# Performance work log

Hardware: AMD Instinct MI355X
Metric: run time of the kernel (lower is better)

The kernel has to match this reference:

```python
import jax, jax.numpy as jnp
import numpy as np

B, L, D, F = 8, 1024, 256, 11
TEMP = D ** 0.5
LN_EPS = 1e-6


def setup_inputs() -> dict:
    key = jax.random.key(0)
    ks = jax.random.split(key, 14)
    mk = lambda k, s: jax.random.normal(k, s, dtype=jnp.float32)
    return {
        "q": mk(ks[0], (B, L, D)),
        "k": mk(ks[1], (B, L, D)),
        "v": mk(ks[2], (B, L, D)),
        "x": jax.random.uniform(ks[3], (B, L, F), dtype=jnp.float32),
        "inputs_lengths": jax.random.randint(ks[4], (B,), 512, L + 1),
        "w_qs": mk(ks[5], (D, D)) * 0.05,
        "w_ks": mk(ks[6], (D, D)) * 0.05,
        "w_vs": mk(ks[7], (D, D)) * 0.05,
        "w_qs2": mk(ks[8], (D, D)) * 0.05,
        "w_ks2": mk(ks[9], (D, D)) * 0.05,
        "w_fc": mk(ks[10], (D, D)) * 0.05,
        "feature_importance": mk(ks[11], (F,)) * 0.1,
        "ln_gamma": jnp.ones((D,), jnp.float32),
        "ln_beta": jnp.zeros((D,), jnp.float32),
    }


def reference(q, k, v, x, w_qs, w_ks, w_vs, w_qs2, w_ks2, w_fc,
              feature_importance, ln_gamma, ln_beta, inputs_lengths):
    lin = lambda a, w: jnp.einsum('bli,oi->blo', a, w)  # torch Linear: y = x W^T
    qp = lin(q, w_qs)
    kp = lin(k, w_ks)
    vp = lin(v, w_vs)
    q2 = lin(q, w_qs2)
    k2 = lin(k, w_ks2)

    # key-position validity mask [B, L]
    key_mask = jnp.arange(L)[None, :] < inputs_lengths[:, None]

    # FeatureSim: pairwise L1 feature distances weighted by feature_importance
    fd = jnp.abs(x[:, :, None, :] - x[:, None, :, :])           # [B,L,L,F]
    fa = jnp.einsum('bijf,f->bij', fd, feature_importance)      # [B,L,L]
    fa = jnp.where(key_mask[:, None, :], fa, -jnp.inf)          # pad_masking
    fa = jax.nn.softmax(fa, axis=-1)
    fa = jnp.nan_to_num(fa)                                     # nan -> 0 for fully-masked rows

    # dual-score attention with tanh activation (no row normalization)
    attn = jnp.einsum('bid,bjd->bij', qp / TEMP, kp)
    q2f = jnp.einsum('bij,bjd->bid', fa, q2)
    k2f = jnp.einsum('bij,bjd->bid', fa, k2)
    attn = attn + jnp.einsum('bid,bjd->bij', q2f / TEMP, k2f)
    zm = key_mask[:, None, :]
    attn = jnp.where(zm, attn, 0.0)                             # pad_zero_masking
    attn = jnp.tanh(attn)
    attn = jnp.where(zm, attn, 0.0)                             # pad_zero_masking (tanh(0)=0, kept for fidelity)

    out = jnp.einsum('bij,bjd->bid', attn, vp)
    out = lin(out, w_fc) + q                                    # dropout is identity at eval
    mu = jnp.mean(out, axis=-1, keepdims=True)
    var = jnp.var(out, axis=-1, keepdims=True)
    out = (out - mu) / jnp.sqrt(var + LN_EPS) * ln_gamma + ln_beta
    return (out, attn)
```

## Files before the change

### kernel.cpp

```cpp
#include <hip/hip_runtime.h>
#include <hip/hip_bf16.h>
#include <math.h>

typedef __hip_bfloat16 bf16;
typedef __bf16 bf16x8 __attribute__((ext_vector_type(8)));
typedef float  f32x4  __attribute__((ext_vector_type(4)));

#define NB 8
#define SL 1024
#define DD 256
#define NF 11
#define RPB 8

#define AS_G __attribute__((address_space(1)))
#define AS_L __attribute__((address_space(3)))

__device__ __forceinline__ bf16x8 ldfrag(const bf16* p) {
  return *reinterpret_cast<const bf16x8*>(p);
}
__device__ __forceinline__ bf16x8 ldfrag(const float* p) {
  const float4 a = *reinterpret_cast<const float4*>(p);
  const float4 b = *reinterpret_cast<const float4*>(p + 4);
  bf16x8 r;
  r[0] = (__bf16)a.x; r[1] = (__bf16)a.y; r[2] = (__bf16)a.z; r[3] = (__bf16)a.w;
  r[4] = (__bf16)b.x; r[5] = (__bf16)b.y; r[6] = (__bf16)b.z; r[7] = (__bf16)b.w;
  return r;
}
__device__ __forceinline__ unsigned short us(float f) {
  bf16 h = __float2bfloat16(f);
  return *reinterpret_cast<unsigned short*>(&h);
}
__device__ __forceinline__ float tanh_fast(float x) {
  return 1.f - 2.f / (__expf(2.f * x) + 1.f);
}

template<int R>
__device__ __forceinline__ void stage_t(const float* __restrict__ g, int ld,
                                        bf16* __restrict__ s, int tid) {
#pragma unroll
  for (int it = 0; it < R / 32; ++it) {
    const int cid = it * 256 + tid;
    const int row = cid >> 3, c16 = cid & 7;
    bf16x8 v = ldfrag(g + (size_t)row * ld + c16 * 8);
    *reinterpret_cast<bf16x8*>(s + row * 64 + ((c16 ^ (row & 7)) << 3)) = v;
  }
}
template<int R>
__device__ __forceinline__ void stage_t(const bf16* __restrict__ g, int ld,
                                        bf16* __restrict__ s, int tid) {
  const int wbase = tid & ~63;
#pragma unroll
  for (int it = 0; it < R / 32; ++it) {
    const int cid = it * 256 + tid;
    const int row = cid >> 3, sc = cid & 7;
    const int c16 = sc ^ (row & 7);
    const bf16* src = g + (size_t)row * ld + c16 * 8;
    bf16* dst = s + (size_t)(it * 256 + wbase) * 8;
    __builtin_amdgcn_global_load_lds((const AS_G void*)src, (AS_L void*)dst, 16, 0, 0);
  }
}

__device__ __forceinline__ void compute_128x128(const bf16* __restrict__ sA,
                                                const bf16* __restrict__ sB,
                                                int lane, int wave, f32x4 acc[4][4]) {
  const int n15 = lane & 15, quad = lane >> 4;
  const int wr = (wave >> 1) << 6, wc = (wave & 1) << 6;
#pragma unroll
  for (int kc = 0; kc < 2; ++kc) {
    const int c16 = kc * 4 + quad;
    bf16x8 aF[4], bF[4];
#pragma unroll
    for (int t = 0; t < 4; ++t) {
      const int ra = wr + t * 16 + n15;
      aF[t] = *reinterpret_cast<const bf16x8*>(sA + ra * 64 + ((c16 ^ (ra & 7)) << 3));
      const int rb = wc + t * 16 + n15;
      bF[t] = *reinterpret_cast<const bf16x8*>(sB + rb * 64 + ((c16 ^ (rb & 7)) << 3));
    }
#pragma unroll
    for (int ti = 0; ti < 4; ++ti)
#pragma unroll
      for (int tj = 0; tj < 4; ++tj)
        acc[ti][tj] = __builtin_amdgcn_mfma_f32_16x16x32_bf16(aF[ti], bF[tj], acc[ti][tj], 0, 0, 0);
  }
}

__device__ __forceinline__ void compute_32x256(const bf16* __restrict__ sA,
                                               const bf16* __restrict__ sB,
                                               int lane, int wave, f32x4 acc[2][4]) {
  const int n15 = lane & 15, quad = lane >> 4;
  const int wc = wave << 6;
#pragma unroll
  for (int kc = 0; kc < 2; ++kc) {
    const int c16 = kc * 4 + quad;
    bf16x8 aF[2], bF[4];
#pragma unroll
    for (int t = 0; t < 2; ++t) {
      const int ra = t * 16 + n15;
      aF[t] = *reinterpret_cast<const bf16x8*>(sA + ra * 64 + ((c16 ^ (ra & 7)) << 3));
    }
#pragma unroll
    for (int t = 0; t < 4; ++t) {
      const int rb = wc + t * 16 + n15;
      bF[t] = *reinterpret_cast<const bf16x8*>(sB + rb * 64 + ((c16 ^ (rb & 7)) << 3));
    }
#pragma unroll
    for (int ti = 0; ti < 2; ++ti)
#pragma unroll
      for (int tj = 0; tj < 4; ++tj)
        acc[ti][tj] = __builtin_amdgcn_mfma_f32_16x16x32_bf16(aF[ti], bF[tj], acc[ti][tj], 0, 0, 0);
  }
}

template<typename TA, typename TB>
__device__ __forceinline__ void gemm_128x128(const TA* __restrict__ A, int lda,
                                             const TB* __restrict__ B, int ldb, int K,
                                             bf16* s, int tid, f32x4 acc[4][4]) {
  const int lane = tid & 63, wave = tid >> 6;
  stage_t<128>(A, lda, s, tid);
  stage_t<128>(B, ldb, s + 8192, tid);
  int cur = 0;
  __syncthreads();
  for (int k0 = 0; k0 < K; k0 += 64) {
    bf16* sc0 = s + cur * 16384;
    if (k0 + 64 < K) {
      bf16* sn = s + (cur ^ 1) * 16384;
      stage_t<128>(A + k0 + 64, lda, sn, tid);
      stage_t<128>(B + k0 + 64, ldb, sn + 8192, tid);
    }
    compute_128x128(sc0, sc0 + 8192, lane, wave, acc);
    __syncthreads();
    cur ^= 1;
  }
}

__device__ __forceinline__ float wred_sum(float v) {
#pragma unroll
  for (int o = 32; o > 0; o >>= 1) v += __shfl_xor(v, o, 64);
  return v;
}

__global__ __launch_bounds__(256) void k_fawc(const float* __restrict__ x,
                                              const float* __restrict__ fi_g,
                                              const int* __restrict__ lens,
                                              const float* __restrict__ wfc,
                                              const float* __restrict__ wvs,
                                              bf16* __restrict__ fa,
                                              float* __restrict__ Wc)
{
  __shared__ __align__(16) float sx[SL * NF];
  __shared__ float sredS[4][RPB];
  const int tid = threadIdx.x, wave = tid >> 6;
  const int bid = blockIdx.x;
  if (bid >= NB * 128) {
    const int o0 = (bid - NB * 128) * 4, m = tid;
    const float* f0 = wfc + (size_t)o0 * DD;
    float a0 = 0.f, a1 = 0.f, a2 = 0.f, a3 = 0.f;
#pragma unroll 8
    for (int i = 0; i < DD; ++i) {
      const float wv = wvs[(size_t)i * DD + m];
      a0 += f0[i] * wv;
      a1 += f0[DD + i] * wv;
      a2 += f0[2 * DD + i] * wv;
      a3 += f0[3 * DD + i] * wv;
    }
    Wc[(size_t)(o0 + 0) * DD + m] = a0;
    Wc[(size_t)(o0 + 1) * DD + m] = a1;
    Wc[(size_t)(o0 + 2) * DD + m] = a2;
    Wc[(size_t)(o0 + 3) * DD + m] = a3;
    return;
  }
  const int b  = bid >> 7;
  const int i0 = (bid & 127) * RPB;
  {
    const float4* src = reinterpret_cast<const float4*>(x + (size_t)b * SL * NF);
    float4* dst = reinterpret_cast<float4*>(sx);
#pragma unroll
    for (int it = 0; it < 11; ++it) dst[it * 256 + tid] = src[it * 256 + tid];
  }
  float fiv[NF];
#pragma unroll
  for (int f = 0; f < NF; ++f) fiv[f] = fi_g[f];
  const int len = lens[b];
  __syncthreads();
  float xi[RPB][NF];
#pragma unroll
  for (int i = 0; i < RPB; ++i)
#pragma unroll
    for (int f = 0; f < NF; ++f) xi[i][f] = sx[(i0 + i) * NF + f];
  float e[RPB][4];
  float ps[RPB];
#pragma unroll
  for (int i = 0; i < RPB; ++i) ps[i] = 0.f;
#pragma unroll
  for (int t = 0; t < 4; ++t) {
    const int j = tid + t * 256;
    const bool valid = (t < 2) || (j < len);
    float xj[NF];
#pragma unroll
    for (int f = 0; f < NF; ++f) xj[f] = sx[j * NF + f];
#pragma unroll
    for (int i = 0; i < RPB; ++i) {
      float a = 0.f;
#pragma unroll
      for (int f = 0; f < NF; ++f) a += fabsf(xi[i][f] - xj[f]) * fiv[f];
      float ev = valid ? __expf(a) : 0.f;
      e[i][t] = ev;
      ps[i] += ev;
    }
  }
#pragma unroll
  for (int i = 0; i < RPB; ++i) {
    float wsv = wred_sum(ps[i]);
    if ((tid & 63) == 0) sredS[wave][i] = wsv;
  }
  __syncthreads();
  bf16* out = fa + (size_t)b * SL * SL + (size_t)i0 * SL;
#pragma unroll
  for (int i = 0; i < RPB; ++i) {
    const float inv = 1.f / (sredS[0][i] + sredS[1][i] + sredS[2][i] + sredS[3][i]);
#pragma unroll
    for (int t = 0; t < 4; ++t)
      out[(size_t)i * SL + tid + t * 256] = __float2bfloat16(e[i][t] * inv);
  }
}

__global__ __launch_bounds__(256) void k_proj(
    const float* __restrict__ q, const float* __restrict__ k, const float* __restrict__ v,
    const float* __restrict__ wqs, const float* __restrict__ wks, const float* __restrict__ Wc,
    const float* __restrict__ wqs2, const float* __restrict__ wks2,
    bf16* __restrict__ qq, bf16* __restrict__ kk,
    bf16* __restrict__ vpwt, bf16* __restrict__ q2t, bf16* __restrict__ k2t)
{
  __shared__ bf16 smem[32768];
  const int tid = threadIdx.x, lane = tid & 63, wave = tid >> 6;
  const int z = blockIdx.z;
  const float* A = (z == 2) ? v : ((z == 1 || z == 4) ? k : q);
  const float* W = (z == 0) ? wqs : (z == 1) ? wks : (z == 2) ? Wc : (z == 3) ? wqs2 : wks2;
  const int rowBase = blockIdx.x * 128;
  const int colBase = blockIdx.y * 128;
  f32x4 acc[4][4] = {};
  gemm_128x128(A + (size_t)rowBase * DD, DD, W + (size_t)colBase * DD, DD, DD, smem, tid, acc);
  const int n15 = lane & 15, quad = lane >> 4;
  const int wr = (wave >> 1) << 6, wc = (wave & 1) << 6;
  if (z <= 1) {
    bf16* O = (z == 0) ? qq : kk;
#pragma unroll
    for (int ti = 0; ti < 4; ++ti)
#pragma unroll
      for (int tj = 0; tj < 4; ++tj)
#pragma unroll
        for (int r = 0; r < 4; ++r) {
          int row = rowBase + wr + ti * 16 + quad * 4 + r;
          int col = colBase + wc + tj * 16 + n15;
          O[(size_t)row * 512 + col] = __float2bfloat16(acc[ti][tj][r]);
        }
  } else {
    bf16* O = (z == 2) ? vpwt : (z == 3) ? q2t : k2t;
    const int bb = rowBase >> 10, rowInB = rowBase & 1023;
#pragma unroll
    for (int ti = 0; ti < 4; ++ti)
#pragma unroll
      for (int tj = 0; tj < 4; ++tj) {
        int l0  = rowInB + wr + ti * 16 + quad * 4;
        int col = colBase + wc + tj * 16 + n15;
        ushort4 pk = make_ushort4(us(acc[ti][tj][0]), us(acc[ti][tj][1]),
                                  us(acc[ti][tj][2]), us(acc[ti][tj][3]));
        *reinterpret_cast<ushort4*>(&O[((size_t)bb * DD + col) * SL + l0]) = pk;
      }
  }
}

__global__ __launch_bounds__(256) void k_famul(const bf16* __restrict__ fa,
                                               const bf16* __restrict__ q2t,
                                               const bf16* __restrict__ k2t,
                                               const int* __restrict__ lens,
                                               bf16* __restrict__ qq,
                                               bf16* __restrict__ kk)
{
  __shared__ bf16 smem[32768];
  const int tid = threadIdx.x, lane = tid & 63, wave = tid >> 6;
  const int flat = blockIdx.x + 8 * blockIdx.y + 16 * blockIdx.z;
  const int lid  = (flat & 7) * 32 + (flat >> 3);
  const int bx = lid & 7, by = (lid >> 3) & 1, bz = lid >> 4;
  const int b = bz >> 1, which = bz & 1;
  const int iBase = bx * 128, dBase = by * 128;
  const int Keff = (lens[b] + 63) & ~63;
  const bf16* A  = fa + (size_t)b * SL * SL + (size_t)iBase * SL;
  const bf16* Bm = (which ? k2t : q2t) + (size_t)b * DD * SL + (size_t)dBase * SL;
  f32x4 acc[4][4] = {};
  gemm_128x128(A, SL, Bm, SL, Keff, smem, tid, acc);
  bf16* O = (which ? kk : qq) + (size_t)b * SL * 512 + 256;
  const int n15 = lane & 15, quad = lane >> 4;
  const int wr = (wave >> 1) << 6, wc = (wave & 1) << 6;
#pragma unroll
  for (int ti = 0; ti < 4; ++ti)
#pragma unroll
    for (int tj = 0; tj < 4; ++tj)
#pragma unroll
      for (int r = 0; r < 4; ++r)
        O[(size_t)(iBase + wr + ti * 16 + quad * 4 + r) * 512 +
          dBase + wc + tj * 16 + n15] = __float2bfloat16(acc[ti][tj][r]);
}

__global__ __launch_bounds__(256) void k_attn(const bf16* __restrict__ qq,
                                              const bf16* __restrict__ kk,
                                              const int* __restrict__ lens,
                                              float* __restrict__ attn_f32,
                                              bf16* __restrict__ attn_b16)
{
  __shared__ bf16 smem[32768];
  const int tid = threadIdx.x, lane = tid & 63, wave = tid >> 6;
  const int flat = blockIdx.x + 8 * blockIdx.y + 64 * blockIdx.z;
  const int lid  = (flat & 7) * 64 + (flat >> 3);
  const int bx = lid & 7, by = (lid >> 3) & 7, bz = lid >> 6;
  const int b = bz;
  const int iBase = bx * 128, jBase = by * 128;
  const int len = lens[b];
  if (jBase >= len) {
    const int r = tid >> 1, ch = (tid & 1) * 64;
    float* pf = attn_f32 + (size_t)b * SL * SL + (size_t)(iBase + r) * SL + jBase + ch;
    bf16*  pb = attn_b16 + (size_t)b * SL * SL + (size_t)(iBase + r) * SL + jBase + ch;
    const float4 z4 = make_float4(0.f, 0.f, 0.f, 0.f);
    const uint4  zb = make_uint4(0u, 0u, 0u, 0u);
#pragma unroll
    for (int i = 0; i < 16; ++i) *reinterpret_cast<float4*>(pf + i * 4) = z4;
#pragma unroll
    for (int i = 0; i < 8; ++i)  *reinterpret_cast<uint4*>(pb + i * 8) = zb;
    return;
  }
  f32x4 acc[4][4] = {};
  gemm_128x128(qq + ((size_t)b * SL + iBase) * 512, 512,
               kk + ((size_t)b * SL + jBase) * 512, 512, 512, smem, tid, acc);
  const int n15 = lane & 15, quad = lane >> 4;
  const int wr = (wave >> 1) << 6, wc = (wave & 1) << 6;
#pragma unroll
  for (int ti = 0; ti < 4; ++ti)
#pragma unroll
    for (int tj = 0; tj < 4; ++tj)
#pragma unroll
      for (int r = 0; r < 4; ++r) {
        int i = iBase + wr + ti * 16 + quad * 4 + r;
        int j = jBase + wc + tj * 16 + n15;
        float vv = (j < len) ? tanh_fast(acc[ti][tj][r] * (1.f / 16.f)) : 0.f;
        size_t idx = (size_t)b * SL * SL + (size_t)i * SL + j;
        attn_f32[idx] = vv;
        attn_b16[idx] = __float2bfloat16(vv);
      }
}

__global__ __launch_bounds__(256) void k_avln(const bf16* __restrict__ attn,
                                              const bf16* __restrict__ vpwt,
                                              const float* __restrict__ qres,
                                              const int* __restrict__ lens,
                                              const float* __restrict__ gam,
                                              const float* __restrict__ bet,
                                              float* __restrict__ outp)
{
  __shared__ bf16 smem[36864];
  const int tid = threadIdx.x, lane = tid & 63, wave = tid >> 6;
  const int flat = blockIdx.x;
  const int lid  = (flat & 7) * 32 + (flat >> 3);
  const int b = lid >> 5, bx = lid & 31;
  const int iBase = bx * 32;
  const int Keff = (lens[b] + 63) & ~63;
  const bf16* A  = attn + (size_t)b * SL * SL + (size_t)iBase * SL;
  const bf16* Bm = vpwt + (size_t)b * DD * SL;
  f32x4 acc[2][4] = {};
  {
    stage_t<32>(A, SL, smem, tid);
    stage_t<256>(Bm, SL, smem + 2048, tid);
    int cur = 0;
    __syncthreads();
    for (int k0 = 0; k0 < Keff; k0 += 64) {
      bf16* sc = smem + cur * 18432;
      if (k0 + 64 < Keff) {
        bf16* sn = smem + (cur ^ 1) * 18432;
        stage_t<32>(A + k0 + 64, SL, sn, tid);
        stage_t<256>(Bm + k0 + 64, SL, sn + 2048, tid);
      }
      compute_32x256(sc, sc + 2048, lane, wave, acc);
      __syncthreads();
      cur ^= 1;
    }
  }
  const int n15 = lane & 15, quad = lane >> 4;
  const int wc = wave << 6;
  float val[2][4][4];
  float sS_p[2][4], sQ_p[2][4];
#pragma unroll
  for (int ti = 0; ti < 2; ++ti)
#pragma unroll
    for (int r = 0; r < 4; ++r) {
      const size_t grow = (size_t)b * SL + iBase + ti * 16 + quad * 4 + r;
      float s = 0.f, ss = 0.f;
#pragma unroll
      for (int tj = 0; tj < 4; ++tj) {
        const int col = wc + tj * 16 + n15;
        float vv = acc[ti][tj][r] + qres[grow * DD + col];
        val[ti][tj][r] = vv;
        s += vv; ss += vv * vv;
      }
      sS_p[ti][r] = s; sQ_p[ti][r] = ss;
    }
#pragma unroll
  for (int o = 8; o > 0; o >>= 1)
#pragma unroll
    for (int ti = 0; ti < 2; ++ti)
#pragma unroll
      for (int r = 0; r < 4; ++r) {
        sS_p[ti][r] += __shfl_xor(sS_p[ti][r], o, 64);
        sQ_p[ti][r] += __shfl_xor(sQ_p[ti][r], o, 64);
      }
  float* sS = (float*)smem;
  float* sQ = sS + 4 * 32;
  if (n15 == 0) {
#pragma unroll
    for (int ti = 0; ti < 2; ++ti)
#pragma unroll
      for (int r = 0; r < 4; ++r) {
        const int rloc = ti * 16 + quad * 4 + r;
        sS[wave * 32 + rloc] = sS_p[ti][r];
        sQ[wave * 32 + rloc] = sQ_p[ti][r];
      }
  }
  __syncthreads();
#pragma unroll
  for (int ti = 0; ti < 2; ++ti)
#pragma unroll
    for (int r = 0; r < 4; ++r) {
      const int rloc = ti * 16 + quad * 4 + r;
      const float s  = sS[rloc] + sS[32 + rloc] + sS[64 + rloc] + sS[96 + rloc];
      const float ss = sQ[rloc] + sQ[32 + rloc] + sQ[64 + rloc] + sQ[96 + rloc];
      const float mean = s * (1.f / DD);
      const float var  = ss * (1.f / DD) - mean * mean;
      const float rstd = rsqrtf(var + 1e-6f);
      const size_t grow = (size_t)b * SL + iBase + rloc;
#pragma unroll
      for (int tj = 0; tj < 4; ++tj) {
        const int col = wc + tj * 16 + n15;
        const float y = (val[ti][tj][r] - mean) * rstd * gam[col] + bet[col];
        outp[grow * DD + col] = y;
      }
    }
}

extern "C" void kernel_launch(void* const* d_in, const int* in_sizes, int n_in,
                              void* d_out, int out_size, void* d_ws, size_t ws_size,
                              hipStream_t stream)
{
  const float* q    = (const float*)d_in[0];
  const float* k    = (const float*)d_in[1];
  const float* v    = (const float*)d_in[2];
  const float* x    = (const float*)d_in[3];
  const int*  lens  = (const int*)d_in[4];
  const float* wqs  = (const float*)d_in[5];
  const float* wks  = (const float*)d_in[6];
  const float* wvs  = (const float*)d_in[7];
  const float* wqs2 = (const float*)d_in[8];
  const float* wks2 = (const float*)d_in[9];
  const float* wfc  = (const float*)d_in[10];
  const float* fi   = (const float*)d_in[11];
  const float* gam  = (const float*)d_in[12];
  const float* bet  = (const float*)d_in[13];

  char* w = (char*)d_ws;
  const size_t MB = 1u << 20;
  bf16* qq    = (bf16*)(w + 0 * MB);
  bf16* kk    = (bf16*)(w + 8 * MB);
  bf16* vpwt  = (bf16*)(w + 16 * MB);
  bf16* q2t   = (bf16*)(w + 20 * MB);
  bf16* k2t   = (bf16*)(w + 24 * MB);
  bf16* fa    = (bf16*)(w + 28 * MB);
  bf16* attn_b16 = fa;
  float* Wc   = (float*)(w + 44 * MB);

  float* outp  = (float*)d_out;
  float* attnp = outp + (size_t)NB * SL * DD;
  (void)wvs;

  dim3 blk(256);
  hipLaunchKernelGGL(k_fawc, dim3(NB * 128 + 64), blk, 0, stream,
                     x, fi, lens, wfc, wvs, fa, Wc);
  hipLaunchKernelGGL(k_proj,  dim3(64, 2, 5),  blk, 0, stream,
                     q, k, v, wqs, wks, Wc, wqs2, wks2, qq, kk, vpwt, q2t, k2t);
  hipLaunchKernelGGL(k_famul, dim3(8, 2, 16),  blk, 0, stream, fa, q2t, k2t, lens, qq, kk);
  hipLaunchKernelGGL(k_attn,  dim3(8, 8, 8),   blk, 0, stream,
                     qq, kk, lens, attnp, attn_b16);
  hipLaunchKernelGGL(k_avln,  dim3(256),       blk, 0, stream,
                     attn_b16, vpwt, q, lens, gam, bet, outp);
}
```

Before: 187.0 us.

## Halve GEMM tile heights and drop double buffering to raise block count

```diff
diff --git a/kernel.cpp b/kernel.cpp
--- a/kernel.cpp
+++ b/kernel.cpp
@@ -59,6 +59,17 @@
     __builtin_amdgcn_global_load_lds((const AS_G void*)src, (AS_L void*)dst, 16, 0, 0);
   }
 }
+__device__ __forceinline__ void stage16(const bf16* __restrict__ g, int ld,
+                                        bf16* __restrict__ s, int tid) {
+  if (tid < 128) {
+    const int wbase = tid & ~63;
+    const int row = tid >> 3, sc = tid & 7;
+    const int c16 = sc ^ (row & 7);
+    const bf16* src = g + (size_t)row * ld + c16 * 8;
+    bf16* dst = s + (size_t)wbase * 8;
+    __builtin_amdgcn_global_load_lds((const AS_G void*)src, (AS_L void*)dst, 16, 0, 0);
+  }
+}
 
 __device__ __forceinline__ void compute_128x128(const bf16* __restrict__ sA,
                                                 const bf16* __restrict__ sB,
@@ -84,18 +95,18 @@
   }
 }
 
-__device__ __forceinline__ void compute_32x256(const bf16* __restrict__ sA,
-                                               const bf16* __restrict__ sB,
-                                               int lane, int wave, f32x4 acc[2][4]) {
-  const int n15 = lane & 15, quad = lane >> 4;
-  const int wc = wave << 6;
+__device__ __forceinline__ void compute_64x128b(const bf16* __restrict__ sA,
+                                                const bf16* __restrict__ sB,
+                                                int lane, int wave, f32x4 acc[2][4]) {
+  const int n15 = lane & 15, quad = lane >> 4;
+  const int wr = (wave >> 1) << 5, wc = (wave & 1) << 6;
 #pragma unroll
   for (int kc = 0; kc < 2; ++kc) {
     const int c16 = kc * 4 + quad;
     bf16x8 aF[2], bF[4];
 #pragma unroll
     for (int t = 0; t < 2; ++t) {
-      const int ra = t * 16 + n15;
+      const int ra = wr + t * 16 + n15;
       aF[t] = *reinterpret_cast<const bf16x8*>(sA + ra * 64 + ((c16 ^ (ra & 7)) << 3));
     }
 #pragma unroll
@@ -108,6 +119,30 @@
 #pragma unroll
       for (int tj = 0; tj < 4; ++tj)
         acc[ti][tj] = __builtin_amdgcn_mfma_f32_16x16x32_bf16(aF[ti], bF[tj], acc[ti][tj], 0, 0, 0);
+  }
+}
+
+__device__ __forceinline__ void compute_16x256(const bf16* __restrict__ sA,
+                                               const bf16* __restrict__ sB,
+                                               int lane, int wave, f32x4 acc[4]) {
+  const int n15 = lane & 15, quad = lane >> 4;
+  const int wc = wave << 6;
+#pragma unroll
+  for (int kc = 0; kc < 2; ++kc) {
+    const int c16 = kc * 4 + quad;
+    bf16x8 aF, bF[4];
+    {
+      const int ra = n15;
+      aF = *reinterpret_cast<const bf16x8*>(sA + ra * 64 + ((c16 ^ (ra & 7)) << 3));
+    }
+#pragma unroll
+    for (int t = 0; t < 4; ++t) {
+      const int rb = wc + t * 16 + n15;
+      bF[t] = *reinterpret_cast<const bf16x8*>(sB + rb * 64 + ((c16 ^ (rb & 7)) << 3));
+    }
+#pragma unroll
+    for (int tj = 0; tj < 4; ++tj)
+      acc[tj] = __builtin_amdgcn_mfma_f32_16x16x32_bf16(aF, bF[tj], acc[tj], 0, 0, 0);
   }
 }
 
@@ -116,20 +151,26 @@
                                              const TB* __restrict__ B, int ldb, int K,
                                              bf16* s, int tid, f32x4 acc[4][4]) {
   const int lane = tid & 63, wave = tid >> 6;
-  stage_t<128>(A, lda, s, tid);
-  stage_t<128>(B, ldb, s + 8192, tid);
-  int cur = 0;
-  __syncthreads();
   for (int k0 = 0; k0 < K; k0 += 64) {
-    bf16* sc0 = s + cur * 16384;
-    if (k0 + 64 < K) {
-      bf16* sn = s + (cur ^ 1) * 16384;
-      stage_t<128>(A + k0 + 64, lda, sn, tid);
-      stage_t<128>(B + k0 + 64, ldb, sn + 8192, tid);
-    }
-    compute_128x128(sc0, sc0 + 8192, lane, wave, acc);
+    stage_t<128>(A + k0, lda, s, tid);
+    stage_t<128>(B + k0, ldb, s + 8192, tid);
     __syncthreads();
-    cur ^= 1;
+    compute_128x128(s, s + 8192, lane, wave, acc);
+    __syncthreads();
+  }
+}
+
+template<typename TA, typename TB>
+__device__ __forceinline__ void gemm_64x128(const TA* __restrict__ A, int lda,
+                                            const TB* __restrict__ B, int ldb, int K,
+                                            bf16* s, int tid, f32x4 acc[2][4]) {
+  const int lane = tid & 63, wave = tid >> 6;
+  for (int k0 = 0; k0 < K; k0 += 64) {
+    stage_t<64>(A + k0, lda, s, tid);
+    stage_t<128>(B + k0, ldb, s + 4096, tid);
+    __syncthreads();
+    compute_64x128b(s, s + 4096, lane, wave, acc);
+    __syncthreads();
   }
 }
 
@@ -231,7 +272,7 @@
     bf16* __restrict__ qq, bf16* __restrict__ kk,
     bf16* __restrict__ vpwt, bf16* __restrict__ q2t, bf16* __restrict__ k2t)
 {
-  __shared__ bf16 smem[32768];
+  __shared__ bf16 smem[16384];
   const int tid = threadIdx.x, lane = tid & 63, wave = tid >> 6;
   const int z = blockIdx.z;
   const float* A = (z == 2) ? v : ((z == 1 || z == 4) ? k : q);
@@ -277,23 +318,23 @@
                                                bf16* __restrict__ qq,
                                                bf16* __restrict__ kk)
 {
-  __shared__ bf16 smem[32768];
+  __shared__ bf16 smem[12288];
   const int tid = threadIdx.x, lane = tid & 63, wave = tid >> 6;
-  const int flat = blockIdx.x + 8 * blockIdx.y + 16 * blockIdx.z;
-  const int lid  = (flat & 7) * 32 + (flat >> 3);
-  const int bx = lid & 7, by = (lid >> 3) & 1, bz = lid >> 4;
-  const int b = bz >> 1, which = bz & 1;
-  const int iBase = bx * 128, dBase = by * 128;
+  const int flat = blockIdx.x;
+  const int lid  = (flat & 7) * 64 + (flat >> 3);
+  const int bx = lid & 15, by = (lid >> 4) & 1;
+  const int which = (lid >> 5) & 1, b = lid >> 6;
+  const int iBase = bx * 64, dBase = by * 128;
   const int Keff = (lens[b] + 63) & ~63;
   const bf16* A  = fa + (size_t)b * SL * SL + (size_t)iBase * SL;
   const bf16* Bm = (which ? k2t : q2t) + (size_t)b * DD * SL + (size_t)dBase * SL;
-  f32x4 acc[4][4] = {};
-  gemm_128x128(A, SL, Bm, SL, Keff, smem, tid, acc);
+  f32x4 acc[2][4] = {};
+  gemm_64x128(A, SL, Bm, SL, Keff, smem, tid, acc);
   bf16* O = (which ? kk : qq) + (size_t)b * SL * 512 + 256;
   const int n15 = lane & 15, quad = lane >> 4;
-  const int wr = (wave >> 1) << 6, wc = (wave & 1) << 6;
-#pragma unroll
-  for (int ti = 0; ti < 4; ++ti)
+  const int wr = (wave >> 1) << 5, wc = (wave & 1) << 6;
+#pragma unroll
+  for (int ti = 0; ti < 2; ++ti)
 #pragma unroll
     for (int tj = 0; tj < 4; ++tj)
 #pragma unroll
@@ -308,33 +349,32 @@
                                               float* __restrict__ attn_f32,
                                               bf16* __restrict__ attn_b16)
 {
-  __shared__ bf16 smem[32768];
+  __shared__ bf16 smem[12288];
   const int tid = threadIdx.x, lane = tid & 63, wave = tid >> 6;
-  const int flat = blockIdx.x + 8 * blockIdx.y + 64 * blockIdx.z;
-  const int lid  = (flat & 7) * 64 + (flat >> 3);
-  const int bx = lid & 7, by = (lid >> 3) & 7, bz = lid >> 6;
-  const int b = bz;
-  const int iBase = bx * 128, jBase = by * 128;
+  const int flat = blockIdx.x;
+  const int lid  = (flat & 7) * 128 + (flat >> 3);
+  const int bx = lid & 15, by = (lid >> 4) & 7, b = lid >> 7;
+  const int iBase = bx * 64, jBase = by * 128;
   const int len = lens[b];
   if (jBase >= len) {
-    const int r = tid >> 1, ch = (tid & 1) * 64;
-    float* pf = attn_f32 + (size_t)b * SL * SL + (size_t)(iBase + r) * SL + jBase + ch;
-    bf16*  pb = attn_b16 + (size_t)b * SL * SL + (size_t)(iBase + r) * SL + jBase + ch;
+    const int r = tid >> 2, c0 = (tid & 3) * 32;
+    float* pf = attn_f32 + (size_t)b * SL * SL + (size_t)(iBase + r) * SL + jBase + c0;
+    bf16*  pb = attn_b16 + (size_t)b * SL * SL + (size_t)(iBase + r) * SL + jBase + c0;
     const float4 z4 = make_float4(0.f, 0.f, 0.f, 0.f);
     const uint4  zb = make_uint4(0u, 0u, 0u, 0u);
 #pragma unroll
-    for (int i = 0; i < 16; ++i) *reinterpret_cast<float4*>(pf + i * 4) = z4;
-#pragma unroll
-    for (int i = 0; i < 8; ++i)  *reinterpret_cast<uint4*>(pb + i * 8) = zb;
+    for (int i = 0; i < 8; ++i) *reinterpret_cast<float4*>(pf + i * 4) = z4;
+#pragma unroll
+    for (int i = 0; i < 4; ++i) *reinterpret_cast<uint4*>(pb + i * 8) = zb;
     return;
   }
-  f32x4 acc[4][4] = {};
-  gemm_128x128(qq + ((size_t)b * SL + iBase) * 512, 512,
-               kk + ((size_t)b * SL + jBase) * 512, 512, 512, smem, tid, acc);
-  const int n15 = lane & 15, quad = lane >> 4;
-  const int wr = (wave >> 1) << 6, wc = (wave & 1) << 6;
-#pragma unroll
-  for (int ti = 0; ti < 4; ++ti)
+  f32x4 acc[2][4] = {};
+  gemm_64x128(qq + ((size_t)b * SL + iBase) * 512, 512,
+              kk + ((size_t)b * SL + jBase) * 512, 512, 512, smem, tid, acc);
+  const int n15 = lane & 15, quad = lane >> 4;
+  const int wr = (wave >> 1) << 5, wc = (wave & 1) << 6;
+#pragma unroll
+  for (int ti = 0; ti < 2; ++ti)
 #pragma unroll
     for (int tj = 0; tj < 4; ++tj)
 #pragma unroll
@@ -356,92 +396,74 @@
                                               const float* __restrict__ bet,
                                               float* __restrict__ outp)
 {
-  __shared__ bf16 smem[36864];
+  __shared__ bf16 smem[17408];
   const int tid = threadIdx.x, lane = tid & 63, wave = tid >> 6;
   const int flat = blockIdx.x;
-  const int lid  = (flat & 7) * 32 + (flat >> 3);
-  const int b = lid >> 5, bx = lid & 31;
-  const int iBase = bx * 32;
+  const int lid  = (flat & 7) * 64 + (flat >> 3);
+  const int b = lid >> 6, bx = lid & 63;
+  const int iBase = bx * 16;
   const int Keff = (lens[b] + 63) & ~63;
   const bf16* A  = attn + (size_t)b * SL * SL + (size_t)iBase * SL;
   const bf16* Bm = vpwt + (size_t)b * DD * SL;
-  f32x4 acc[2][4] = {};
-  {
-    stage_t<32>(A, SL, smem, tid);
-    stage_t<256>(Bm, SL, smem + 2048, tid);
-    int cur = 0;
+  f32x4 acc[4] = {};
+  for (int k0 = 0; k0 < Keff; k0 += 64) {
+    stage16(A + k0, SL, smem, tid);
+    stage_t<256>(Bm + k0, SL, smem + 1024, tid);
     __syncthreads();
-    for (int k0 = 0; k0 < Keff; k0 += 64) {
-      bf16* sc = smem + cur * 18432;
-      if (k0 + 64 < Keff) {
-        bf16* sn = smem + (cur ^ 1) * 18432;
-        stage_t<32>(A + k0 + 64, SL, sn, tid);
-        stage_t<256>(Bm + k0 + 64, SL, sn + 2048, tid);
-      }
-      compute_32x256(sc, sc + 2048, lane, wave, acc);
-      __syncthreads();
-      cur ^= 1;
-    }
+    compute_16x256(smem, smem + 1024, lane, wave, acc);
+    __syncthreads();
   }
   const int n15 = lane & 15, quad = lane >> 4;
   const int wc = wave << 6;
-  float val[2][4][4];
-  float sS_p[2][4], sQ_p[2][4];
-#pragma unroll
-  for (int ti = 0; ti < 2; ++ti)
+  float val[4][4];
+  float sS_p[4], sQ_p[4];
+#pragma unroll
+  for (int r = 0; r < 4; ++r) {
+    const size_t grow = (size_t)b * SL + iBase + quad * 4 + r;
+    float s = 0.f, ss = 0.f;
+#pragma unroll
+    for (int tj = 0; tj < 4; ++tj) {
+      const int col = wc + tj * 16 + n15;
+      float vv = acc[tj][r] + qres[grow * DD + col];
+      val[tj][r] = vv;
+      s += vv; ss += vv * vv;
+    }
+    sS_p[r] = s; sQ_p[r] = ss;
+  }
+#pragma unroll
+  for (int o = 8; o > 0; o >>= 1)
 #pragma unroll
     for (int r = 0; r < 4; ++r) {
-      const size_t grow = (size_t)b * SL + iBase + ti * 16 + quad * 4 + r;
-      float s = 0.f, ss = 0.f;
-#pragma unroll
-      for (int tj = 0; tj < 4; ++tj) {
-        const int col = wc + tj * 16 + n15;
-        float vv = acc[ti][tj][r] + qres[grow * DD + col];
-        val[ti][tj][r] = vv;
-        s += vv; ss += vv * vv;
-      }
-      sS_p[ti][r] = s; sQ_p[ti][r] = ss;
-    }
-#pragma unroll
-  for (int o = 8; o > 0; o >>= 1)
-#pragma unroll
-    for (int ti = 0; ti < 2; ++ti)
-#pragma unroll
-      for (int r = 0; r < 4; ++r) {
-        sS_p[ti][r] += __shfl_xor(sS_p[ti][r], o, 64);
-        sQ_p[ti][r] += __shfl_xor(sQ_p[ti][r], o, 64);
-      }
+      sS_p[r] += __shfl_xor(sS_p[r], o, 64);
+      sQ_p[r] += __shfl_xor(sQ_p[r], o, 64);
+    }
   float* sS = (float*)smem;
-  float* sQ = sS + 4 * 32;
+  float* sQ = sS + 4 * 16;
   if (n15 == 0) {
 #pragma unroll
-    for (int ti = 0; ti < 2; ++ti)
-#pragma unroll
-      for (int r = 0; r < 4; ++r) {
-        const int rloc = ti * 16 + quad * 4 + r;
-        sS[wave * 32 + rloc] = sS_p[ti][r];
-        sQ[wave * 32 + rloc] = sQ_p[ti][r];
-      }
+    for (int r = 0; r < 4; ++r) {
+      const int rloc = quad * 4 + r;
+      sS[wave * 16 + rloc] = sS_p[r];
+      sQ[wave * 16 + rloc] = sQ_p[r];
+    }
   }
   __syncthreads();
 #pragma unroll
-  for (int ti = 0; ti < 2; ++ti)
-#pragma unroll
-    for (int r = 0; r < 4; ++r) {
-      const int rloc = ti * 16 + quad * 4 + r;
-      const float s  = sS[rloc] + sS[32 + rloc] + sS[64 + rloc] + sS[96 + rloc];
-      const float ss = sQ[rloc] + sQ[32 + rloc] + sQ[64 + rloc] + sQ[96 + rloc];
-      const float mean = s * (1.f / DD);
-      const float var  = ss * (1.f / DD) - mean * mean;
-      const float rstd = rsqrtf(var + 1e-6f);
-      const size_t grow = (size_t)b * SL + iBase + rloc;
-#pragma unroll
-      for (int tj = 0; tj < 4; ++tj) {
-        const int col = wc + tj * 16 + n15;
-        const float y = (val[ti][tj][r] - mean) * rstd * gam[col] + bet[col];
-        outp[grow * DD + col] = y;
-      }
-    }
+  for (int r = 0; r < 4; ++r) {
+    const int rloc = quad * 4 + r;
+    const float s  = sS[rloc] + sS[16 + rloc] + sS[32 + rloc] + sS[48 + rloc];
+    const float ss = sQ[rloc] + sQ[16 + rloc] + sQ[32 + rloc] + sQ[48 + rloc];
+    const float mean = s * (1.f / DD);
+    const float var  = ss * (1.f / DD) - mean * mean;
+    const float rstd = rsqrtf(var + 1e-6f);
+    const size_t grow = (size_t)b * SL + iBase + rloc;
+#pragma unroll
+    for (int tj = 0; tj < 4; ++tj) {
+      const int col = wc + tj * 16 + n15;
+      const float y = (val[tj][r] - mean) * rstd * gam[col] + bet[col];
+      outp[grow * DD + col] = y;
+    }
+  }
 }
 
 extern "C" void kernel_launch(void* const* d_in, const int* in_sizes, int n_in,
@@ -483,9 +505,9 @@
                      x, fi, lens, wfc, wvs, fa, Wc);
   hipLaunchKernelGGL(k_proj,  dim3(64, 2, 5),  blk, 0, stream,
                      q, k, v, wqs, wks, Wc, wqs2, wks2, qq, kk, vpwt, q2t, k2t);
-  hipLaunchKernelGGL(k_famul, dim3(8, 2, 16),  blk, 0, stream, fa, q2t, k2t, lens, qq, kk);
-  hipLaunchKernelGGL(k_attn,  dim3(8, 8, 8),   blk, 0, stream,
+  hipLaunchKernelGGL(k_famul, dim3(512),       blk, 0, stream, fa, q2t, k2t, lens, qq, kk);
+  hipLaunchKernelGGL(k_attn,  dim3(1024),      blk, 0, stream,
                      qq, kk, lens, attnp, attn_b16);
-  hipLaunchKernelGGL(k_avln,  dim3(256),       blk, 0, stream,
+  hipLaunchKernelGGL(k_avln,  dim3(512),       blk, 0, stream,
                      attn_b16, vpwt, q, lens, gam, bet, outp);
 }
```

After: 190.5 us. No clear change (+1.9%).

## Merge projection and feature-softmax kernels; apply fc weight inside AV+LayerNorm kernel

Applied to the files above, without the earlier changes.

```diff
diff --git a/kernel.cpp b/kernel.cpp
--- a/kernel.cpp
+++ b/kernel.cpp
@@ -139,38 +139,64 @@
   return v;
 }
 
-__global__ __launch_bounds__(256) void k_fawc(const float* __restrict__ x,
-                                              const float* __restrict__ fi_g,
-                                              const int* __restrict__ lens,
-                                              const float* __restrict__ wfc,
-                                              const float* __restrict__ wvs,
-                                              bf16* __restrict__ fa,
-                                              float* __restrict__ Wc)
+__global__ __launch_bounds__(256) void k_fp(
+    const float* __restrict__ q, const float* __restrict__ k, const float* __restrict__ v,
+    const float* __restrict__ x, const float* __restrict__ fi_g,
+    const int* __restrict__ lens,
+    const float* __restrict__ wqs, const float* __restrict__ wks,
+    const float* __restrict__ wvs, const float* __restrict__ wqs2,
+    const float* __restrict__ wks2,
+    bf16* __restrict__ qq, bf16* __restrict__ kk,
+    bf16* __restrict__ vpt, bf16* __restrict__ q2t, bf16* __restrict__ k2t,
+    bf16* __restrict__ fa)
 {
-  __shared__ __align__(16) float sx[SL * NF];
-  __shared__ float sredS[4][RPB];
-  const int tid = threadIdx.x, wave = tid >> 6;
+  __shared__ __align__(16) char pool[65536];
+  const int tid = threadIdx.x, lane = tid & 63, wave = tid >> 6;
   const int bid = blockIdx.x;
-  if (bid >= NB * 128) {
-    const int o0 = (bid - NB * 128) * 4, m = tid;
-    const float* f0 = wfc + (size_t)o0 * DD;
-    float a0 = 0.f, a1 = 0.f, a2 = 0.f, a3 = 0.f;
-#pragma unroll 8
-    for (int i = 0; i < DD; ++i) {
-      const float wv = wvs[(size_t)i * DD + m];
-      a0 += f0[i] * wv;
-      a1 += f0[DD + i] * wv;
-      a2 += f0[2 * DD + i] * wv;
-      a3 += f0[3 * DD + i] * wv;
-    }
-    Wc[(size_t)(o0 + 0) * DD + m] = a0;
-    Wc[(size_t)(o0 + 1) * DD + m] = a1;
-    Wc[(size_t)(o0 + 2) * DD + m] = a2;
-    Wc[(size_t)(o0 + 3) * DD + m] = a3;
+  if (bid < 640) {
+    bf16* smem = (bf16*)pool;
+    const int z = bid >> 7, sub = bid & 127;
+    const int rowBase = (sub & 63) * 128;
+    const int colBase = (sub >> 6) * 128;
+    const float* A = (z == 2) ? v : ((z == 1 || z == 4) ? k : q);
+    const float* W = (z == 0) ? wqs : (z == 1) ? wks : (z == 2) ? wvs : (z == 3) ? wqs2 : wks2;
+    f32x4 acc[4][4] = {};
+    gemm_128x128(A + (size_t)rowBase * DD, DD, W + (size_t)colBase * DD, DD, DD, smem, tid, acc);
+    const int n15 = lane & 15, quad = lane >> 4;
+    const int wr = (wave >> 1) << 6, wc = (wave & 1) << 6;
+    if (z <= 1) {
+      bf16* O = (z == 0) ? qq : kk;
+#pragma unroll
+      for (int ti = 0; ti < 4; ++ti)
+#pragma unroll
+        for (int tj = 0; tj < 4; ++tj)
+#pragma unroll
+          for (int r = 0; r < 4; ++r) {
+            int row = rowBase + wr + ti * 16 + quad * 4 + r;
+            int col = colBase + wc + tj * 16 + n15;
+            O[(size_t)row * 512 + col] = __float2bfloat16(acc[ti][tj][r]);
+          }
+    } else {
+      bf16* O = (z == 2) ? vpt : (z == 3) ? q2t : k2t;
+      const int bb = rowBase >> 10, rowInB = rowBase & 1023;
+#pragma unroll
+      for (int ti = 0; ti < 4; ++ti)
+#pragma unroll
+        for (int tj = 0; tj < 4; ++tj) {
+          int l0  = rowInB + wr + ti * 16 + quad * 4;
+          int col = colBase + wc + tj * 16 + n15;
+          ushort4 pk = make_ushort4(us(acc[ti][tj][0]), us(acc[ti][tj][1]),
+                                    us(acc[ti][tj][2]), us(acc[ti][tj][3]));
+          *reinterpret_cast<ushort4*>(&O[((size_t)bb * DD + col) * SL + l0]) = pk;
+        }
+    }
     return;
   }
-  const int b  = bid >> 7;
-  const int i0 = (bid & 127) * RPB;
+  float* sx = (float*)pool;
+  float* sredS = (float*)(pool + 45056);
+  const int fid = bid - 640;
+  const int b  = fid >> 7;
+  const int i0 = (fid & 127) * RPB;
   {
     const float4* src = reinterpret_cast<const float4*>(x + (size_t)b * SL * NF);
     float4* dst = reinterpret_cast<float4*>(sx);
@@ -211,62 +237,17 @@
 #pragma unroll
   for (int i = 0; i < RPB; ++i) {
     float wsv = wred_sum(ps[i]);
-    if ((tid & 63) == 0) sredS[wave][i] = wsv;
+    if ((tid & 63) == 0) sredS[wave * RPB + i] = wsv;
   }
   __syncthreads();
   bf16* out = fa + (size_t)b * SL * SL + (size_t)i0 * SL;
 #pragma unroll
   for (int i = 0; i < RPB; ++i) {
-    const float inv = 1.f / (sredS[0][i] + sredS[1][i] + sredS[2][i] + sredS[3][i]);
+    const float inv = 1.f / (sredS[0 * RPB + i] + sredS[1 * RPB + i] +
+                             sredS[2 * RPB + i] + sredS[3 * RPB + i]);
 #pragma unroll
     for (int t = 0; t < 4; ++t)
       out[(size_t)i * SL + tid + t * 256] = __float2bfloat16(e[i][t] * inv);
-  }
-}
-
-__global__ __launch_bounds__(256) void k_proj(
-    const float* __restrict__ q, const float* __restrict__ k, const float* __restrict__ v,
-    const float* __restrict__ wqs, const float* __restrict__ wks, const float* __restrict__ Wc,
-    const float* __restrict__ wqs2, const float* __restrict__ wks2,
-    bf16* __restrict__ qq, bf16* __restrict__ kk,
-    bf16* __restrict__ vpwt, bf16* __restrict__ q2t, bf16* __restrict__ k2t)
-{
-  __shared__ bf16 smem[32768];
-  const int tid = threadIdx.x, lane = tid & 63, wave = tid >> 6;
-  const int z = blockIdx.z;
-  const float* A = (z == 2) ? v : ((z == 1 || z == 4) ? k : q);
-  const float* W = (z == 0) ? wqs : (z == 1) ? wks : (z == 2) ? Wc : (z == 3) ? wqs2 : wks2;
-  const int rowBase = blockIdx.x * 128;
-  const int colBase = blockIdx.y * 128;
-  f32x4 acc[4][4] = {};
-  gemm_128x128(A + (size_t)rowBase * DD, DD, W + (size_t)colBase * DD, DD, DD, smem, tid, acc);
-  const int n15 = lane & 15, quad = lane >> 4;
-  const int wr = (wave >> 1) << 6, wc = (wave & 1) << 6;
-  if (z <= 1) {
-    bf16* O = (z == 0) ? qq : kk;
-#pragma unroll
-    for (int ti = 0; ti < 4; ++ti)
-#pragma unroll
-      for (int tj = 0; tj < 4; ++tj)
-#pragma unroll
-        for (int r = 0; r < 4; ++r) {
-          int row = rowBase + wr + ti * 16 + quad * 4 + r;
-          int col = colBase + wc + tj * 16 + n15;
-          O[(size_t)row * 512 + col] = __float2bfloat16(acc[ti][tj][r]);
-        }
-  } else {
-    bf16* O = (z == 2) ? vpwt : (z == 3) ? q2t : k2t;
-    const int bb = rowBase >> 10, rowInB = rowBase & 1023;
-#pragma unroll
-    for (int ti = 0; ti < 4; ++ti)
-#pragma unroll
-      for (int tj = 0; tj < 4; ++tj) {
-        int l0  = rowInB + wr + ti * 16 + quad * 4;
-        int col = colBase + wc + tj * 16 + n15;
-        ushort4 pk = make_ushort4(us(acc[ti][tj][0]), us(acc[ti][tj][1]),
-                                  us(acc[ti][tj][2]), us(acc[ti][tj][3]));
-        *reinterpret_cast<ushort4*>(&O[((size_t)bb * DD + col) * SL + l0]) = pk;
-      }
   }
 }
 
@@ -349,8 +330,9 @@
 }
 
 __global__ __launch_bounds__(256) void k_avln(const bf16* __restrict__ attn,
-                                              const bf16* __restrict__ vpwt,
+                                              const bf16* __restrict__ vpt,
                                               const float* __restrict__ qres,
+                                              const float* __restrict__ wfc,
                                               const int* __restrict__ lens,
                                               const float* __restrict__ gam,
                                               const float* __restrict__ bet,
@@ -364,7 +346,7 @@
   const int iBase = bx * 32;
   const int Keff = (lens[b] + 63) & ~63;
   const bf16* A  = attn + (size_t)b * SL * SL + (size_t)iBase * SL;
-  const bf16* Bm = vpwt + (size_t)b * DD * SL;
+  const bf16* Bm = vpt + (size_t)b * DD * SL;
   f32x4 acc[2][4] = {};
   {
     stage_t<32>(A, SL, smem, tid);
@@ -384,7 +366,32 @@
     }
   }
   const int n15 = lane & 15, quad = lane >> 4;
-  const int wc = wave << 6;
+  bf16* sY  = smem;
+  bf16* sB2 = smem + 8192;
+#pragma unroll
+  for (int ti = 0; ti < 2; ++ti)
+#pragma unroll
+    for (int tj = 0; tj < 4; ++tj)
+#pragma unroll
+      for (int r = 0; r < 4; ++r) {
+        const int row = ti * 16 + quad * 4 + r;
+        const int cc  = tj * 16 + n15;
+        sY[wave * 2048 + row * 64 + (((cc >> 3) ^ (row & 7)) << 3) + (cc & 7)] =
+            __float2bfloat16(acc[ti][tj][r]);
+      }
+  stage_t<256>(wfc, DD, sB2, tid);
+  __syncthreads();
+  f32x4 acc2[2][4] = {};
+#pragma unroll 1
+  for (int kb = 0; kb < 4; ++kb) {
+    compute_32x256(sY + kb * 2048, sB2, lane, wave, acc2);
+    __syncthreads();
+    if (kb < 3) {
+      stage_t<256>(wfc + (kb + 1) * 64, DD, sB2, tid);
+      __syncthreads();
+    }
+  }
+  const int wcol = wave << 6;
   float val[2][4][4];
   float sS_p[2][4], sQ_p[2][4];
 #pragma unroll
@@ -395,8 +402,8 @@
       float s = 0.f, ss = 0.f;
 #pragma unroll
       for (int tj = 0; tj < 4; ++tj) {
-        const int col = wc + tj * 16 + n15;
-        float vv = acc[ti][tj][r] + qres[grow * DD + col];
+        const int col = wcol + tj * 16 + n15;
+        float vv = acc2[ti][tj][r] + qres[grow * DD + col];
         val[ti][tj][r] = vv;
         s += vv; ss += vv * vv;
       }
@@ -437,7 +444,7 @@
       const size_t grow = (size_t)b * SL + iBase + rloc;
 #pragma unroll
       for (int tj = 0; tj < 4; ++tj) {
-        const int col = wc + tj * 16 + n15;
+        const int col = wcol + tj * 16 + n15;
         const float y = (val[ti][tj][r] - mean) * rstd * gam[col] + bet[col];
         outp[grow * DD + col] = y;
       }
@@ -467,25 +474,22 @@
   const size_t MB = 1u << 20;
   bf16* qq    = (bf16*)(w + 0 * MB);
   bf16* kk    = (bf16*)(w + 8 * MB);
-  bf16* vpwt  = (bf16*)(w + 16 * MB);
+  bf16* vpt   = (bf16*)(w + 16 * MB);
   bf16* q2t   = (bf16*)(w + 20 * MB);
   bf16* k2t   = (bf16*)(w + 24 * MB);
   bf16* fa    = (bf16*)(w + 28 * MB);
   bf16* attn_b16 = fa;
-  float* Wc   = (float*)(w + 44 * MB);
 
   float* outp  = (float*)d_out;
   float* attnp = outp + (size_t)NB * SL * DD;
-  (void)wvs;
 
   dim3 blk(256);
-  hipLaunchKernelGGL(k_fawc, dim3(NB * 128 + 64), blk, 0, stream,
-                     x, fi, lens, wfc, wvs, fa, Wc);
-  hipLaunchKernelGGL(k_proj,  dim3(64, 2, 5),  blk, 0, stream,
-                     q, k, v, wqs, wks, Wc, wqs2, wks2, qq, kk, vpwt, q2t, k2t);
+  hipLaunchKernelGGL(k_fp,    dim3(640 + NB * 128), blk, 0, stream,
+                     q, k, v, x, fi, lens, wqs, wks, wvs, wqs2, wks2,
+                     qq, kk, vpt, q2t, k2t, fa);
   hipLaunchKernelGGL(k_famul, dim3(8, 2, 16),  blk, 0, stream, fa, q2t, k2t, lens, qq, kk);
   hipLaunchKernelGGL(k_attn,  dim3(8, 8, 8),   blk, 0, stream,
                      qq, kk, lens, attnp, attn_b16);
   hipLaunchKernelGGL(k_avln,  dim3(256),       blk, 0, stream,
-                     attn_b16, vpwt, q, lens, gam, bet, outp);
-}
+                     attn_b16, vpt, q, wfc, lens, gam, bet, outp);
+}
```

New measurement: 182.0 us. -2.7%, faster.
